# Optimization experiments

Measured on AMD Instinct MI355X. Metric: run time of the kernel, lower is better.

The kernel has to match this reference:

```python
import jax, jax.numpy as jnp
import numpy as np

B, D, N, H = 4, 1024, 2048, 16
HD = D // H  # head dim = 64


def rotate_half(x):
    # pairs (x1, x2) -> (-x2, x1), interleaved along last dim
    x1 = x[..., 0::2]
    x2 = x[..., 1::2]
    return jnp.stack((-x2, x1), axis=-1).reshape(x.shape)


def apply_cached_rotary_emb(freqs, t):
    return t * freqs[0] + rotate_half(t) * freqs[1]


def setup_inputs() -> dict:
    key = jax.random.key(0)
    ks = jax.random.split(key, 13)
    s = 1.0 / np.sqrt(D)
    inp = {
        "query": jax.random.normal(ks[0], (B, D, N), jnp.float32),
        "key": jax.random.normal(ks[1], (B, D, N), jnp.float32),
        "value": jax.random.normal(ks[2], (B, D, N), jnp.float32),
        "encoding": jax.random.normal(ks[3], (2, 1, 1, N, HD), jnp.float32),
        "Wq": jax.random.normal(ks[4], (D, D), jnp.float32) * s,
        "bq": jax.random.normal(ks[5], (D,), jnp.float32) * s,
        "Wk": jax.random.normal(ks[6], (D, D), jnp.float32) * s,
        "bk": jax.random.normal(ks[7], (D,), jnp.float32) * s,
        "Wv": jax.random.normal(ks[8], (D, D), jnp.float32) * s,
        "bv": jax.random.normal(ks[9], (D,), jnp.float32) * s,
        "Wm": jax.random.normal(ks[10], (D, D), jnp.float32) * s,
        "bm": jax.random.normal(ks[11], (D,), jnp.float32) * s,
    }
    return inp


def reference(query, key, value, encoding, Wq, bq, Wk, bk, Wv, bv, Wm, bm):
    b, d_model, n = query.shape

    def proj(W, bias, x):  # Conv1d with kernel_size=1 == pointwise matmul
        return jnp.einsum('oi,bin->bon', W, x) + bias[None, :, None]

    # [B, D, N] -> [B, HD, H, N]  (channel split: dim-major, as in .view(B, dim, H, -1))
    q = proj(Wq, bq, query).reshape(b, HD, H, n)
    k = proj(Wk, bk, key).reshape(b, HD, H, n)
    v = proj(Wv, bv, value).reshape(b, HD, H, n)

    # RoPE applied in [B, H, N, HD] layout, then back to [B, HD, H, N]
    q = jnp.transpose(apply_cached_rotary_emb(encoding, jnp.transpose(q, (0, 2, 3, 1))), (0, 3, 1, 2))
    k = jnp.transpose(apply_cached_rotary_emb(encoding, jnp.transpose(k, (0, 2, 3, 1))), (0, 3, 1, 2))

    scores = jnp.einsum('bdhn,bdhm->bhnm', q, k) / np.float32(np.sqrt(HD))
    prob = jax.nn.softmax(scores, axis=-1)
    x = jnp.einsum('bhnm,bdhm->bdhn', prob, v)

    out = jnp.einsum('oi,bin->bon', Wm, x.reshape(b, d_model, n)) + bm[None, :, None]
    return out
```

## Files before the change

kernel.cpp:

```cpp
#include <hip/hip_runtime.h>
#include <hip/hip_bf16.h>

typedef __bf16 bf16;
typedef __bf16 bf16x8 __attribute__((ext_vector_type(8)));
typedef __bf16 bf16x4 __attribute__((ext_vector_type(4)));
typedef float f32x4 __attribute__((ext_vector_type(4)));
typedef unsigned int uint4v __attribute__((ext_vector_type(4)));
typedef unsigned int uint2v __attribute__((ext_vector_type(2)));

#define LOG2E 1.44269504088896340736f

typedef __attribute__((address_space(1))) const unsigned int guint;
typedef __attribute__((address_space(3))) unsigned int luint;

__device__ __forceinline__ void gload_lds16(const bf16* g, bf16* l) {
  __builtin_amdgcn_global_load_lds((guint*)g, (luint*)l, 16, 0, 0);
}

__global__ __launch_bounds__(256) void k_transpose3(const float* __restrict__ q,
                                                    const float* __restrict__ k,
                                                    const float* __restrict__ v,
                                                    bf16* __restrict__ tq,
                                                    bf16* __restrict__ tk,
                                                    bf16* __restrict__ tv) {
  __shared__ bf16 T[64][72];
  const int t = threadIdx.x;
  const int n0 = blockIdx.x * 64;
  const int i0 = blockIdx.y * 64;
  const int z = blockIdx.z;
  const int b = z & 3, which = z >> 2;
  const float* src = (which == 0) ? q : ((which == 1) ? k : v);
  bf16* dst = (which == 0) ? tq : ((which == 1) ? tk : tv);
  const size_t srcb = (size_t)b * 1024 * 2048;
#pragma unroll
  for (int p = 0; p < 2; ++p) {
    int idx = p * 256 + t;
    int row = idx >> 3;
    int seg = idx & 7;
    const float* sp = src + srcb + (size_t)(i0 + row) * 2048 + n0 + seg * 8;
    f32x4 a = *(const f32x4*)sp;
    f32x4 c = *(const f32x4*)(sp + 4);
    bf16x8 o;
#pragma unroll
    for (int e = 0; e < 4; ++e) { o[e] = (bf16)a[e]; o[4 + e] = (bf16)c[e]; }
    *(bf16x8*)&T[row][seg * 8] = o;
  }
  __syncthreads();
  const int j = t >> 2;
  const int iseg = t & 3;
  bf16x8 o0, o1;
#pragma unroll
  for (int e = 0; e < 8; ++e) o0[e] = T[iseg * 16 + e][j];
#pragma unroll
  for (int e = 0; e < 8; ++e) o1[e] = T[iseg * 16 + 8 + e][j];
  bf16* dp = dst + (size_t)b * 2048 * 1024 + (size_t)(n0 + j) * 1024 + i0 + iseg * 16;
  *(bf16x8*)dp = o0;
  *(bf16x8*)(dp + 8) = o1;
}

__global__ __launch_bounds__(512, 4) void k_gemm3(const bf16* __restrict__ Wqb,
                                                  const bf16* __restrict__ Wkb,
                                                  const bf16* __restrict__ Wvb,
                                                  const float* __restrict__ bq,
                                                  const float* __restrict__ bk,
                                                  const float* __restrict__ bv,
                                                  const bf16* __restrict__ tq,
                                                  const bf16* __restrict__ tk,
                                                  const bf16* __restrict__ tv,
                                                  bf16* __restrict__ qp,
                                                  bf16* __restrict__ kp,
                                                  bf16* __restrict__ vp) {
  const int K = 1024, Nn = 2048;
  const int z = blockIdx.z;
  const int b = z & 3, which = z >> 2;
  const bf16* A = (which == 0) ? Wqb : ((which == 1) ? Wkb : Wvb);
  const bf16* Bt = (which == 0) ? tq : ((which == 1) ? tk : tv);
  const float* bias = (which == 0) ? bq : ((which == 1) ? bk : bv);
  bf16* C = (which == 0) ? qp : ((which == 1) ? kp : vp);

  __shared__ bf16 As[256 * 64];
  __shared__ bf16 Bs[128 * 64];
  const int t = threadIdx.x;
  const int w = t >> 6, l = t & 63, q = l >> 4, li = l & 15;
  const int o0 = blockIdx.y * 256, n0 = blockIdx.x * 128;
  const bf16* Ab = A + (size_t)o0 * K;
  const bf16* Bb = Bt + (size_t)b * Nn * K + (size_t)n0 * K;
  const int wr = (w >> 1) * 64, wc = (w & 1) * 64;
  f32x4 acc[4][4];
#pragma unroll
  for (int i = 0; i < 4; ++i)
#pragma unroll
    for (int j = 0; j < 4; ++j) acc[i][j] = (f32x4){0.f, 0.f, 0.f, 0.f};

  int srow[4], sseg[4];
#pragma unroll
  for (int p = 0; p < 4; ++p) {
    int ci = p * 512 + t;
    srow[p] = ci >> 3;
    sseg[p] = ((ci & 7) ^ (srow[p] & 7)) * 8;
  }
  const int swz = li & 7;

  for (int k0 = 0; k0 < K; k0 += 64) {
    __syncthreads();
#pragma unroll
    for (int p = 0; p < 4; ++p)
      gload_lds16(Ab + (size_t)srow[p] * K + k0 + sseg[p], As + (size_t)(p * 512 + w * 64) * 8);
#pragma unroll
    for (int p = 0; p < 2; ++p)
      gload_lds16(Bb + (size_t)srow[p] * K + k0 + sseg[p], Bs + (size_t)(p * 512 + w * 64) * 8);
    __syncthreads();
#pragma unroll
    for (int kk = 0; kk < 2; ++kk) {
      const int cc = ((kk * 4 + q) ^ swz) * 8;
      bf16x8 af[4], bfr[4];
#pragma unroll
      for (int mt = 0; mt < 4; ++mt) af[mt] = *(const bf16x8*)&As[(wr + mt * 16 + li) * 64 + cc];
#pragma unroll
      for (int c = 0; c < 4; ++c) bfr[c] = *(const bf16x8*)&Bs[(wc + c * 16 + li) * 64 + cc];
#pragma unroll
      for (int mt = 0; mt < 4; ++mt)
#pragma unroll
        for (int c = 0; c < 4; ++c)
          acc[mt][c] = __builtin_amdgcn_mfma_f32_16x16x32_bf16(af[mt], bfr[c], acc[mt][c], 0, 0, 0);
    }
  }

  bf16* Cb = C + (size_t)b * K * Nn;
#pragma unroll
  for (int mt = 0; mt < 4; ++mt) {
#pragma unroll
    for (int r = 0; r < 4; ++r) {
      int o = o0 + wr + mt * 16 + q * 4 + r;
      float bvv = bias[o];
#pragma unroll
      for (int c = 0; c < 4; ++c) {
        int n = n0 + wc + c * 16 + li;
        Cb[(size_t)o * Nn + n] = (bf16)(acc[mt][c][r] + bvv);
      }
    }
  }
}

template <typename OT>
__global__ __launch_bounds__(256) void k_gemm(const bf16* __restrict__ A,
                                              const bf16* __restrict__ Bt,
                                              const float* __restrict__ bias,
                                              OT* __restrict__ C,
                                              int M, int K, int Nn) {
  __shared__ bf16 As[128 * 64];
  __shared__ bf16 Bs[128 * 64];
  const int t = threadIdx.x;
  const int w = t >> 6, l = t & 63, q = l >> 4, li = l & 15;
  const int o0 = blockIdx.y * 128, n0 = blockIdx.x * 128;
  const int b = blockIdx.z;
  const bf16* Ab = A + (size_t)o0 * K;
  const bf16* Bb = Bt + (size_t)b * Nn * K + (size_t)n0 * K;
  const int wr = (w >> 1) * 64, wc = (w & 1) * 64;
  f32x4 acc[4][4];
#pragma unroll
  for (int i = 0; i < 4; ++i)
#pragma unroll
    for (int j = 0; j < 4; ++j) acc[i][j] = (f32x4){0.f, 0.f, 0.f, 0.f};

  int srow[4], sseg[4];
#pragma unroll
  for (int p = 0; p < 4; ++p) {
    int ci = p * 256 + t;
    srow[p] = ci >> 3;
    sseg[p] = ((ci & 7) ^ (srow[p] & 7)) * 8;
  }
  const int swz = li & 7;

  for (int k0 = 0; k0 < K; k0 += 64) {
    __syncthreads();
#pragma unroll
    for (int p = 0; p < 4; ++p) {
      gload_lds16(Ab + (size_t)srow[p] * K + k0 + sseg[p], As + (size_t)(p * 256 + w * 64) * 8);
      gload_lds16(Bb + (size_t)srow[p] * K + k0 + sseg[p], Bs + (size_t)(p * 256 + w * 64) * 8);
    }
    __syncthreads();
#pragma unroll
    for (int kk = 0; kk < 2; ++kk) {
      const int cc = ((kk * 4 + q) ^ swz) * 8;
      bf16x8 af[4], bfr[4];
#pragma unroll
      for (int mt = 0; mt < 4; ++mt) af[mt] = *(const bf16x8*)&As[(wr + mt * 16 + li) * 64 + cc];
#pragma unroll
      for (int c = 0; c < 4; ++c) bfr[c] = *(const bf16x8*)&Bs[(wc + c * 16 + li) * 64 + cc];
#pragma unroll
      for (int mt = 0; mt < 4; ++mt)
#pragma unroll
        for (int c = 0; c < 4; ++c)
          acc[mt][c] = __builtin_amdgcn_mfma_f32_16x16x32_bf16(af[mt], bfr[c], acc[mt][c], 0, 0, 0);
    }
  }

  OT* Cb = C + (size_t)b * M * Nn;
#pragma unroll
  for (int mt = 0; mt < 4; ++mt) {
#pragma unroll
    for (int r = 0; r < 4; ++r) {
      int o = o0 + wr + mt * 16 + q * 4 + r;
      float bv = bias[o];
#pragma unroll
      for (int c = 0; c < 4; ++c) {
        int n = n0 + wc + c * 16 + li;
        Cb[(size_t)o * Nn + n] = (OT)(acc[mt][c][r] + bv);
      }
    }
  }
}

__global__ __launch_bounds__(256) void k_rope2(const bf16* __restrict__ qp,
                                               const bf16* __restrict__ kp,
                                               const float* __restrict__ enc,
                                               bf16* __restrict__ qa,
                                               bf16* __restrict__ ka) {
  __shared__ bf16 T[64][72];
  const int t = threadIdx.x;
  const int n0 = blockIdx.x * 64;
  const int h = blockIdx.y;
  const int z = blockIdx.z;
  const int b = z & 3, which = z >> 2;
  const bf16* src = which ? kp : qp;
  bf16* dst = which ? ka : qa;
  const float oscale = which ? 1.0f : 0.125f * LOG2E;
#pragma unroll
  for (int p = 0; p < 2; ++p) {
    int idx = p * 256 + t;
    int hd = idx >> 3;
    int seg = idx & 7;
    *(bf16x8*)&T[hd][seg * 8] =
        *(const bf16x8*)(src + (size_t)(b * 1024 + hd * 16 + h) * 2048 + n0 + seg * 8);
  }
  __syncthreads();
  const int j = t >> 2;
  const int hd0 = (t & 3) * 16;
  const int n = n0 + j;
  const float* e0 = enc + (size_t)n * 64 + hd0;
  const float* e1 = enc + (size_t)2048 * 64 + (size_t)n * 64 + hd0;
  bf16x8 o0, o1;
#pragma unroll
  for (int i = 0; i < 8; ++i) {
    int e = 2 * i;
    float t0 = (float)T[hd0 + e][j];
    float t1 = (float)T[hd0 + e + 1][j];
    float f00 = e0[e], f01 = e0[e + 1];
    float f10 = e1[e], f11 = e1[e + 1];
    float r0 = (t0 * f00 - t1 * f10) * oscale;
    float r1 = (t1 * f01 + t0 * f11) * oscale;
    if (i < 4) { o0[e & 7] = (bf16)r0; o0[(e & 7) + 1] = (bf16)r1; }
    else       { o1[e & 7] = (bf16)r0; o1[(e & 7) + 1] = (bf16)r1; }
  }
  bf16* dp = dst + ((size_t)(b * 16 + h) * 2048 + n) * 64 + hd0;
  *(bf16x8*)dp = o0;
  *(bf16x8*)(dp + 8) = o1;
}

__global__ __launch_bounds__(512, 4) void k_attn(const bf16* __restrict__ qa,
                                                 const bf16* __restrict__ ka,
                                                 const bf16* __restrict__ vp,
                                                 bf16* __restrict__ xo) {
  __shared__ bf16 Ks[64 * 72];
  __shared__ bf16 Vs[64 * 72];
  const int t = threadIdx.x;
  const int w = t >> 6, l = t & 63, q = l >> 4, li = l & 15;
  const int n0 = blockIdx.x * 256, h = blockIdx.y, b = blockIdx.z;
  const bool oddrow = ((t >> 4) & 1) != 0;
  const bf16* Qb = qa + (size_t)(b * 16 + h) * 2048 * 64;
  const bf16* Kb = ka + (size_t)(b * 16 + h) * 2048 * 64;
  const bf16* Vb = vp + (size_t)b * 1024 * 2048 + (size_t)h * 2048;

  const int r0 = t >> 3, s0 = (t & 7) * 8;

  bf16x8 qf[2][2];
#pragma unroll
  for (int bt = 0; bt < 2; ++bt)
#pragma unroll
    for (int kk = 0; kk < 2; ++kk)
      qf[bt][kk] = *(const bf16x8*)(Qb + (size_t)(n0 + w * 32 + bt * 16 + li) * 64 + kk * 32 + q * 8);

  bf16x8 onef;
#pragma unroll
  for (int e = 0; e < 8; ++e) onef[e] = (bf16)1.0f;

  f32x4 acc[4][2];
#pragma unroll
  for (int i = 0; i < 4; ++i)
#pragma unroll
    for (int j = 0; j < 2; ++j) acc[i][j] = (f32x4){0.f, 0.f, 0.f, 0.f};
  f32x4 accl[2] = {(f32x4){0.f, 0.f, 0.f, 0.f}, (f32x4){0.f, 0.f, 0.f, 0.f}};

  bf16x8 kr0, vr0;
  kr0 = *(const bf16x8*)(Kb + (size_t)r0 * 64 + s0);
  vr0 = *(const bf16x8*)(Vb + (size_t)r0 * 32768 + s0);
  *(bf16x8*)&Ks[r0 * 72 + s0] = kr0;
  *(bf16x8*)&Vs[r0 * 72 + s0] = vr0;
  __syncthreads();

  for (int m0 = 0; m0 < 2048; m0 += 64) {
    const int mn = (m0 + 64 < 2048) ? m0 + 64 : m0;
    kr0 = *(const bf16x8*)(Kb + (size_t)(mn + r0) * 64 + s0);
    vr0 = *(const bf16x8*)(Vb + (size_t)r0 * 32768 + mn + s0);

    f32x4 sacc[4][2];
#pragma unroll
    for (int mt = 0; mt < 4; ++mt)
#pragma unroll
      for (int bt = 0; bt < 2; ++bt) sacc[mt][bt] = (f32x4){0.f, 0.f, 0.f, 0.f};
#pragma unroll
    for (int kk = 0; kk < 2; ++kk) {
#pragma unroll
      for (int mt = 0; mt < 4; ++mt) {
        bf16x8 af = *(const bf16x8*)&Ks[(mt * 16 + li) * 72 + kk * 32 + q * 8];
#pragma unroll
        for (int bt = 0; bt < 2; ++bt)
          sacc[mt][bt] = __builtin_amdgcn_mfma_f32_16x16x32_bf16(af, qf[bt][kk], sacc[mt][bt], 0, 0, 0);
      }
    }

    unsigned pk32[2][4][2];
#pragma unroll
    for (int mt = 0; mt < 4; ++mt)
#pragma unroll
      for (int bt = 0; bt < 2; ++bt) {
        bf16x4 pk;
#pragma unroll
        for (int r = 0; r < 4; ++r) pk[r] = (bf16)__builtin_amdgcn_exp2f(sacc[mt][bt][r]);
        uint2v pu = __builtin_bit_cast(uint2v, pk);
        pk32[bt][mt][0] = pu[0];
        pk32[bt][mt][1] = pu[1];
      }

#pragma unroll
    for (int kk = 0; kk < 2; ++kk) {
      bf16x8 pf[2];
#pragma unroll
      for (int bt = 0; bt < 2; ++bt) {
        uint4v du;
#pragma unroll
        for (int hh = 0; hh < 2; ++hh) {
          unsigned p0 = pk32[bt][2 * kk + 0][hh];
          unsigned p1 = pk32[bt][2 * kk + 1][hh];
          uint2v ab = __builtin_amdgcn_permlane32_swap(p0, p1, false, false);
          unsigned A = ab[0];
          unsigned Bv = ab[1];
          unsigned swzA = (unsigned)__builtin_amdgcn_ds_swizzle((int)A, 0x401F);
          unsigned swzB = (unsigned)__builtin_amdgcn_ds_swizzle((int)Bv, 0x401F);
          du[hh]     = oddrow ? swzB : A;
          du[2 + hh] = oddrow ? Bv : swzA;
        }
        pf[bt] = __builtin_bit_cast(bf16x8, du);
        accl[bt] = __builtin_amdgcn_mfma_f32_16x16x32_bf16(onef, pf[bt], accl[bt], 0, 0, 0);
      }
#pragma unroll
      for (int hdt = 0; hdt < 4; ++hdt) {
        bf16x8 vf = *(const bf16x8*)&Vs[(hdt * 16 + li) * 72 + kk * 32 + q * 8];
#pragma unroll
        for (int bt = 0; bt < 2; ++bt)
          acc[hdt][bt] = __builtin_amdgcn_mfma_f32_16x16x32_bf16(vf, pf[bt], acc[hdt][bt], 0, 0, 0);
      }
    }

    __syncthreads();
    *(bf16x8*)&Ks[r0 * 72 + s0] = kr0;
    *(bf16x8*)&Vs[r0 * 72 + s0] = vr0;
    __syncthreads();
  }

  float inv[2] = {1.0f / accl[0][0], 1.0f / accl[1][0]};

  bf16* xb = xo + (size_t)b * 2048 * 1024 + (size_t)h * 64;
#pragma unroll
  for (int hdt = 0; hdt < 4; ++hdt)
#pragma unroll
    for (int bt = 0; bt < 2; ++bt) {
      int n = n0 + w * 32 + bt * 16 + li;
      bf16x4 o;
#pragma unroll
      for (int r = 0; r < 4; ++r) o[r] = (bf16)(acc[hdt][bt][r] * inv[bt]);
      *(bf16x4*)(xb + (size_t)n * 1024 + hdt * 16 + q * 4) = o;
    }
}

__global__ __launch_bounds__(256) void k_prepw(const float* __restrict__ Wq,
                                               const float* __restrict__ Wk,
                                               const float* __restrict__ Wv,
                                               const float* __restrict__ Wm,
                                               bf16* __restrict__ oq,
                                               bf16* __restrict__ ok,
                                               bf16* __restrict__ ov,
                                               bf16* __restrict__ om) {
  const int which = blockIdx.y;
  if (which < 3) {
    const float* s = (which == 0) ? Wq : ((which == 1) ? Wk : Wv);
    bf16* d = (which == 0) ? oq : ((which == 1) ? ok : ov);
    int idx = (blockIdx.x * 256 + threadIdx.x) * 4;
    f32x4 a = *(const f32x4*)(s + idx);
    bf16x4 o;
#pragma unroll
    for (int e = 0; e < 4; ++e) o[e] = (bf16)a[e];
    *(bf16x4*)(d + idx) = o;
  } else {
#pragma unroll
    for (int p = 0; p < 4; ++p) {
      int idx = (blockIdx.x * 4 + p) * 256 + threadIdx.x;
      int o = idx >> 10, j = idx & 1023;
      int hd = j & 63, hh = j >> 6;
      om[idx] = (bf16)Wm[((size_t)o << 10) + (size_t)(hd * 16 + hh)];
    }
  }
}

extern "C" void kernel_launch(void* const* d_in, const int* in_sizes, int n_in,
                              void* d_out, int out_size, void* d_ws, size_t ws_size,
                              hipStream_t stream) {
  const float* query = (const float*)d_in[0];
  const float* key   = (const float*)d_in[1];
  const float* value = (const float*)d_in[2];
  const float* enc   = (const float*)d_in[3];
  const float* Wq = (const float*)d_in[4];  const float* bq = (const float*)d_in[5];
  const float* Wk = (const float*)d_in[6];  const float* bk = (const float*)d_in[7];
  const float* Wv = (const float*)d_in[8];  const float* bv = (const float*)d_in[9];
  const float* Wm = (const float*)d_in[10]; const float* bm = (const float*)d_in[11];

  char* ws = (char*)d_ws;
  const size_t SZ = (size_t)4 * 2048 * 1024 * 2;
  const size_t WZ = (size_t)1024 * 1024 * 2;
  bf16* bufA = (bf16*)(ws + 0 * SZ);
  bf16* bufB = (bf16*)(ws + 1 * SZ);
  bf16* bufC = (bf16*)(ws + 2 * SZ);
  bf16* bufD = (bf16*)(ws + 3 * SZ);
  bf16* Wqb  = (bf16*)(ws + 4 * SZ + 0 * WZ);
  bf16* Wkb  = (bf16*)(ws + 4 * SZ + 1 * WZ);
  bf16* Wvb  = (bf16*)(ws + 4 * SZ + 2 * WZ);
  bf16* Wmp  = (bf16*)(ws + 4 * SZ + 3 * WZ);
  bf16* vt   = (bf16*)d_out;
  bf16* vpd  = (bf16*)d_out + (size_t)4 * 2048 * 1024;

  dim3 blk(256);
  k_prepw<<<dim3(1024, 4), blk, 0, stream>>>(Wq, Wk, Wv, Wm, Wqb, Wkb, Wvb, Wmp);
  k_transpose3<<<dim3(32, 16, 12), blk, 0, stream>>>(query, key, value, bufA, bufB, vt);
  k_gemm3<<<dim3(16, 4, 12), dim3(512), 0, stream>>>(Wqb, Wkb, Wvb, bq, bk, bv,
                                                     bufA, bufB, vt, bufC, bufD, vpd);
  k_rope2<<<dim3(32, 16, 8), blk, 0, stream>>>(bufC, bufD, enc, bufA, bufB);
  k_attn<<<dim3(8, 16, 4), dim3(512), 0, stream>>>(bufA, bufB, vpd, bufC);
  k_gemm<float><<<dim3(16, 8, 4), blk, 0, stream>>>(Wmp, bufC, bm, (float*)d_out, 1024, 1024, 2048);
}
```

Before: 350.0 us.

## Double-buffer QKV projection GEMM with 256x256 tiles and interleaved load/MFMA phases

Rewrites the fused QKV projection GEMM to use 256x256 output tiles per block, double-buffered LDS (As0/As1, Bs0/Bs1), and a four-phase schedule. Each phase issues the next tile's global-to-LDS loads, then runs a quarter of the MFMAs under raised wave priority. The goal is to hide global-load latency behind compute and raise arithmetic intensity per block. In exchange it uses far more LDS (128 KB) and more accumulator registers, drops occupancy to 2 blocks per CU, and halves the grid to 384 blocks.

```diff
diff --git a/kernel.cpp b/kernel.cpp
--- a/kernel.cpp
+++ b/kernel.cpp
@@ -58,7 +58,74 @@
   *(bf16x8*)(dp + 8) = o1;
 }
 
-__global__ __launch_bounds__(512, 4) void k_gemm3(const bf16* __restrict__ Wqb,
+#define G3_BAR() do { __builtin_amdgcn_s_barrier(); __builtin_amdgcn_sched_barrier(0); \
+                      asm volatile("" ::: "memory"); } while (0)
+
+#define G3_TILE(AC, BC, AN, BN, KN) do {                                                   \
+    bf16x8 bA[4][2], bB[4][2];                                                             \
+                   \
+    gload_lds16(Ag0 + (KN), (AN) + (size_t)(0 * 512 + w * 64) * 8);                        \
+    gload_lds16(Bg0 + (KN), (BN) + (size_t)(0 * 512 + w * 64) * 8);                        \
+    _Pragma("unroll") for (int i = 0; i < 4; ++i)                                          \
+      _Pragma("unroll") for (int kk = 0; kk < 2; ++kk)                                     \
+        bA[i][kk] = *(const bf16x8*)&(AC)[(wr + i * 16 + li) * 64 + ((kk * 4 + q) ^ swz) * 8]; \
+    _Pragma("unroll") for (int c = 0; c < 2; ++c)                                          \
+      _Pragma("unroll") for (int kk = 0; kk < 2; ++kk)                                     \
+        bB[c][kk] = *(const bf16x8*)&(BC)[(wc + c * 16 + li) * 64 + ((kk * 4 + q) ^ swz) * 8]; \
+    G3_BAR();                                                                              \
+    __builtin_amdgcn_s_setprio(1);                                                         \
+    _Pragma("unroll") for (int i = 0; i < 4; ++i)                                          \
+      _Pragma("unroll") for (int c = 0; c < 2; ++c)                                        \
+        _Pragma("unroll") for (int kk = 0; kk < 2; ++kk)                                   \
+          acc[i][c] = __builtin_amdgcn_mfma_f32_16x16x32_bf16(bA[i][kk], bB[c][kk], acc[i][c], 0, 0, 0); \
+    __builtin_amdgcn_s_setprio(0);                                                         \
+    G3_BAR();                                                                              \
+                              \
+    gload_lds16(Ag1 + (KN), (AN) + (size_t)(1 * 512 + w * 64) * 8);                        \
+    gload_lds16(Bg1 + (KN), (BN) + (size_t)(1 * 512 + w * 64) * 8);                        \
+    _Pragma("unroll") for (int c = 0; c < 2; ++c)                                          \
+      _Pragma("unroll") for (int kk = 0; kk < 2; ++kk)                                     \
+        bB[2 + c][kk] = *(const bf16x8*)&(BC)[(wc + (2 + c) * 16 + li) * 64 + ((kk * 4 + q) ^ swz) * 8]; \
+    G3_BAR();                                                                              \
+    __builtin_amdgcn_s_setprio(1);                                                         \
+    _Pragma("unroll") for (int i = 0; i < 4; ++i)                                          \
+      _Pragma("unroll") for (int c = 0; c < 2; ++c)                                        \
+        _Pragma("unroll") for (int kk = 0; kk < 2; ++kk)                                   \
+          acc[i][2 + c] = __builtin_amdgcn_mfma_f32_16x16x32_bf16(bA[i][kk], bB[2 + c][kk], acc[i][2 + c], 0, 0, 0); \
+    __builtin_amdgcn_s_setprio(0);                                                         \
+    G3_BAR();                                                                              \
+                              \
+    gload_lds16(Ag2 + (KN), (AN) + (size_t)(2 * 512 + w * 64) * 8);                        \
+    gload_lds16(Bg2 + (KN), (BN) + (size_t)(2 * 512 + w * 64) * 8);                        \
+    _Pragma("unroll") for (int i = 0; i < 4; ++i)                                          \
+      _Pragma("unroll") for (int kk = 0; kk < 2; ++kk)                                     \
+        bA[i][kk] = *(const bf16x8*)&(AC)[(wr + (4 + i) * 16 + li) * 64 + ((kk * 4 + q) ^ swz) * 8]; \
+    G3_BAR();                                                                              \
+    __builtin_amdgcn_s_setprio(1);                                                         \
+    _Pragma("unroll") for (int i = 0; i < 4; ++i)                                          \
+      _Pragma("unroll") for (int c = 0; c < 2; ++c)                                        \
+        _Pragma("unroll") for (int kk = 0; kk < 2; ++kk)                                   \
+          acc[4 + i][2 + c] = __builtin_amdgcn_mfma_f32_16x16x32_bf16(bA[i][kk], bB[2 + c][kk], acc[4 + i][2 + c], 0, 0, 0); \
+    __builtin_amdgcn_s_setprio(0);                                                         \
+    G3_BAR();                                                                              \
+        \
+    gload_lds16(Ag3 + (KN), (AN) + (size_t)(3 * 512 + w * 64) * 8);                        \
+    gload_lds16(Bg3 + (KN), (BN) + (size_t)(3 * 512 + w * 64) * 8);                        \
+    G3_BAR();                                                                              \
+    __builtin_amdgcn_s_setprio(1);                                                         \
+    _Pragma("unroll") for (int i = 0; i < 4; ++i)                                          \
+      _Pragma("unroll") for (int c = 0; c < 2; ++c)                                        \
+        _Pragma("unroll") for (int kk = 0; kk < 2; ++kk)                                   \
+          acc[4 + i][c] = __builtin_amdgcn_mfma_f32_16x16x32_bf16(bA[i][kk], bB[c][kk], acc[4 + i][c], 0, 0, 0); \
+    __builtin_amdgcn_s_setprio(0);                                                         \
+    asm volatile("s_waitcnt vmcnt(0)" ::: "memory");                                       \
+    __builtin_amdgcn_sched_barrier(0);                                                     \
+    __builtin_amdgcn_s_barrier();                                                          \
+    __builtin_amdgcn_sched_barrier(0);                                                     \
+    asm volatile("" ::: "memory");                                                         \
+  } while (0)
+
+__global__ __launch_bounds__(512, 2) void k_gemm3(const bf16* __restrict__ Wqb,
                                                   const bf16* __restrict__ Wkb,
                                                   const bf16* __restrict__ Wvb,
                                                   const float* __restrict__ bq,
@@ -78,57 +145,61 @@
   const float* bias = (which == 0) ? bq : ((which == 1) ? bk : bv);
   bf16* C = (which == 0) ? qp : ((which == 1) ? kp : vp);
 
-  __shared__ bf16 As[256 * 64];
-  __shared__ bf16 Bs[128 * 64];
+  __shared__ bf16 As0[256 * 64], Bs0[256 * 64];
+  __shared__ bf16 As1[256 * 64], Bs1[256 * 64];
   const int t = threadIdx.x;
   const int w = t >> 6, l = t & 63, q = l >> 4, li = l & 15;
-  const int o0 = blockIdx.y * 256, n0 = blockIdx.x * 128;
+  const int o0 = blockIdx.y * 256, n0 = blockIdx.x * 256;
   const bf16* Ab = A + (size_t)o0 * K;
   const bf16* Bb = Bt + (size_t)b * Nn * K + (size_t)n0 * K;
-  const int wr = (w >> 1) * 64, wc = (w & 1) * 64;
-  f32x4 acc[4][4];
-#pragma unroll
-  for (int i = 0; i < 4; ++i)
+  const int wr = (w >> 2) * 128, wc = (w & 3) * 64;
+  f32x4 acc[8][4];
+#pragma unroll
+  for (int i = 0; i < 8; ++i)
 #pragma unroll
     for (int j = 0; j < 4; ++j) acc[i][j] = (f32x4){0.f, 0.f, 0.f, 0.f};
 
-  int srow[4], sseg[4];
+  int srow_[4], sseg_[4];
 #pragma unroll
   for (int p = 0; p < 4; ++p) {
     int ci = p * 512 + t;
-    srow[p] = ci >> 3;
-    sseg[p] = ((ci & 7) ^ (srow[p] & 7)) * 8;
-  }
+    srow_[p] = ci >> 3;
+    sseg_[p] = ((ci & 7) ^ (srow_[p] & 7)) * 8;
+  }
+  const bf16* Ag0 = Ab + (size_t)srow_[0] * K + sseg_[0];
+  const bf16* Ag1 = Ab + (size_t)srow_[1] * K + sseg_[1];
+  const bf16* Ag2 = Ab + (size_t)srow_[2] * K + sseg_[2];
+  const bf16* Ag3 = Ab + (size_t)srow_[3] * K + sseg_[3];
+  const bf16* Bg0 = Bb + (size_t)srow_[0] * K + sseg_[0];
+  const bf16* Bg1 = Bb + (size_t)srow_[1] * K + sseg_[1];
+  const bf16* Bg2 = Bb + (size_t)srow_[2] * K + sseg_[2];
+  const bf16* Bg3 = Bb + (size_t)srow_[3] * K + sseg_[3];
   const int swz = li & 7;
 
-  for (int k0 = 0; k0 < K; k0 += 64) {
-    __syncthreads();
-#pragma unroll
-    for (int p = 0; p < 4; ++p)
-      gload_lds16(Ab + (size_t)srow[p] * K + k0 + sseg[p], As + (size_t)(p * 512 + w * 64) * 8);
-#pragma unroll
-    for (int p = 0; p < 2; ++p)
-      gload_lds16(Bb + (size_t)srow[p] * K + k0 + sseg[p], Bs + (size_t)(p * 512 + w * 64) * 8);
-    __syncthreads();
-#pragma unroll
-    for (int kk = 0; kk < 2; ++kk) {
-      const int cc = ((kk * 4 + q) ^ swz) * 8;
-      bf16x8 af[4], bfr[4];
-#pragma unroll
-      for (int mt = 0; mt < 4; ++mt) af[mt] = *(const bf16x8*)&As[(wr + mt * 16 + li) * 64 + cc];
-#pragma unroll
-      for (int c = 0; c < 4; ++c) bfr[c] = *(const bf16x8*)&Bs[(wc + c * 16 + li) * 64 + cc];
-#pragma unroll
-      for (int mt = 0; mt < 4; ++mt)
-#pragma unroll
-        for (int c = 0; c < 4; ++c)
-          acc[mt][c] = __builtin_amdgcn_mfma_f32_16x16x32_bf16(af[mt], bfr[c], acc[mt][c], 0, 0, 0);
-    }
+  gload_lds16(Ag0, As0 + (size_t)(0 * 512 + w * 64) * 8);
+  gload_lds16(Bg0, Bs0 + (size_t)(0 * 512 + w * 64) * 8);
+  gload_lds16(Ag1, As0 + (size_t)(1 * 512 + w * 64) * 8);
+  gload_lds16(Bg1, Bs0 + (size_t)(1 * 512 + w * 64) * 8);
+  gload_lds16(Ag2, As0 + (size_t)(2 * 512 + w * 64) * 8);
+  gload_lds16(Bg2, Bs0 + (size_t)(2 * 512 + w * 64) * 8);
+  gload_lds16(Ag3, As0 + (size_t)(3 * 512 + w * 64) * 8);
+  gload_lds16(Bg3, Bs0 + (size_t)(3 * 512 + w * 64) * 8);
+  asm volatile("s_waitcnt vmcnt(0)" ::: "memory");
+  __builtin_amdgcn_s_barrier();
+  __builtin_amdgcn_sched_barrier(0);
+  asm volatile("" ::: "memory");
+
+#pragma unroll 1
+  for (int k0 = 0; k0 < K; k0 += 128) {
+    const int k1 = k0 + 64;
+    const int k2 = (k0 + 128 < K) ? (k0 + 128) : 0;
+    G3_TILE(As0, Bs0, As1, Bs1, k1);
+    G3_TILE(As1, Bs1, As0, Bs0, k2);
   }
 
   bf16* Cb = C + (size_t)b * K * Nn;
 #pragma unroll
-  for (int mt = 0; mt < 4; ++mt) {
+  for (int mt = 0; mt < 8; ++mt) {
 #pragma unroll
     for (int r = 0; r < 4; ++r) {
       int o = o0 + wr + mt * 16 + q * 4 + r;
@@ -442,8 +513,8 @@
   dim3 blk(256);
   k_prepw<<<dim3(1024, 4), blk, 0, stream>>>(Wq, Wk, Wv, Wm, Wqb, Wkb, Wvb, Wmp);
   k_transpose3<<<dim3(32, 16, 12), blk, 0, stream>>>(query, key, value, bufA, bufB, vt);
-  k_gemm3<<<dim3(16, 4, 12), dim3(512), 0, stream>>>(Wqb, Wkb, Wvb, bq, bk, bv,
-                                                     bufA, bufB, vt, bufC, bufD, vpd);
+  k_gemm3<<<dim3(8, 4, 12), dim3(512), 0, stream>>>(Wqb, Wkb, Wvb, bq, bk, bv,
+                                                    bufA, bufB, vt, bufC, bufD, vpd);
   k_rope2<<<dim3(32, 16, 8), blk, 0, stream>>>(bufC, bufD, enc, bufA, bufB);
   k_attn<<<dim3(8, 16, 4), dim3(512), 0, stream>>>(bufA, bufB, vpd, bufC);
   k_gemm<float><<<dim3(16, 8, 4), blk, 0, stream>>>(Wmp, bufC, bm, (float*)d_out, 1024, 1024, 2048);
```

Result: slower. 367.9 us (+5.1%).
